# Performance work log

Hardware: AMD Instinct MI355X
Metric: run time of the kernel (lower is better)

The kernel has to match this reference:

```python
import jax, jax.numpy as jnp
import numpy as np
import math

N_HEAD = 32
ROPE_BASE = 10000.0


def _rope_headwise(x):
    # Faithful to the source bug: x is [B, H, S, D] and the rotary module uses
    # x.shape[1] (= H) as the "sequence length", so the angle depends on the
    # head index, broadcast over the true sequence axis.
    B, H, S, D = x.shape
    inv_freq = 1.0 / (ROPE_BASE ** (jnp.arange(0, D, 2, dtype=jnp.float32) / D))  # [D/2]
    t = jnp.arange(H, dtype=jnp.float32)                                          # [H]
    freqs = t[:, None] * inv_freq[None, :]                                        # [H, D/2]
    # emb = cat(freqs, freqs)[..., :D//2] == freqs, so cos/sin are just over freqs
    cos = jnp.cos(freqs)[None, :, None, :]   # [1, H, 1, D/2]
    sin = jnp.sin(freqs)[None, :, None, :]
    x1, x2 = x[..., : D // 2], x[..., D // 2 :]
    return jnp.concatenate([x1 * cos - x2 * sin, x1 * sin + x2 * cos], axis=-1)


def setup_inputs() -> dict:
    key = jax.random.key(0)
    ks = jax.random.split(key, 5)
    B, S, E = 2, 2048, 2048
    scale = 0.02
    return {
        "x": jax.random.normal(ks[0], (B, S, E), dtype=jnp.float32),
        "Wq": jax.random.normal(ks[1], (E, E), dtype=jnp.float32) * scale,
        "bq": jnp.zeros((E,), dtype=jnp.float32),
        "Wk": jax.random.normal(ks[2], (E, E), dtype=jnp.float32) * scale,
        "bk": jnp.zeros((E,), dtype=jnp.float32),
        "Wv": jax.random.normal(ks[3], (E, E), dtype=jnp.float32) * scale,
        "bv": jnp.zeros((E,), dtype=jnp.float32),
        "Wo": jax.random.normal(ks[4], (E, E), dtype=jnp.float32) * scale,
        "bo": jnp.zeros((E,), dtype=jnp.float32),
    }


def reference(x, Wq, bq, Wk, bk, Wv, bv, Wo, bo):
    B, S, E = x.shape
    H = N_HEAD
    D = E // H

    def split_heads(y):  # [B,S,E] -> [B,H,S,D]
        return y.reshape(B, S, H, D).transpose(0, 2, 1, 3)

    q = split_heads(x @ Wq + bq)
    k = split_heads(x @ Wk + bk)
    v = split_heads(x @ Wv + bv)

    q = _rope_headwise(q)
    k = _rope_headwise(k)

    scores = jnp.einsum("bhqd,bhkd->bhqk", q, k) / math.sqrt(D)  # [B,H,S,S]
    causal = jnp.triu(jnp.ones((S, S), dtype=bool), k=1)
    scores = jnp.where(causal[None, None], -jnp.inf, scores)
    attn = jax.nn.softmax(scores, axis=-1)
    out = jnp.einsum("bhqk,bhkd->bhqd", attn, v)                 # [B,H,S,D]
    out = out.transpose(0, 2, 1, 3).reshape(B, S, E)
    return out @ Wo + bo
```

## Files before the change

### kernel.cpp

```cpp
#include <hip/hip_runtime.h>
#include <hip/hip_bf16.h>

#define B_ 2
#define S_ 2048
#define E_ 2048
#define H_ 32
#define M_ (B_*S_)

typedef __bf16 bf16x8 __attribute__((ext_vector_type(8)));
typedef float  f32x4  __attribute__((ext_vector_type(4)));

__device__ __forceinline__ ushort f2bf(float f) {
    uint u = __float_as_uint(f);
    u += 0x7fffu + ((u >> 16) & 1u);
    return (ushort)(u >> 16);
}
__device__ __forceinline__ uint pack2bf(float a, float b) {
    __hip_bfloat162 h = __float22bfloat162_rn(make_float2(a, b));
    return *(uint*)&h;
}
__device__ __forceinline__ float bf2f(ushort h) {
    return __uint_as_float(((uint)h) << 16);
}
__device__ __forceinline__ f32x4 f4zero() {
    f32x4 z; z[0]=0.f; z[1]=0.f; z[2]=0.f; z[3]=0.f; return z;
}
__device__ __forceinline__ void async16(const ushort* g, ushort* l) {
    __builtin_amdgcn_global_load_lds((const __attribute__((address_space(1))) void*)g,
                                     (__attribute__((address_space(3))) void*)l, 16, 0, 0);
}

__global__ __launch_bounds__(256) void cast_x_kernel(const float* __restrict__ x,
                                                     ushort* __restrict__ xb) {
    int i = (blockIdx.x * 256 + threadIdx.x) * 4;
    float4 v = *(const float4*)(x + i);
    uint2 o;
    o.x = pack2bf(v.x, v.y);
    o.y = pack2bf(v.z, v.w);
    *(uint2*)(xb + i) = o;
}

__global__ __launch_bounds__(256) void wtrans_kernel(const float* __restrict__ W0, const float* __restrict__ W1,
                                                     const float* __restrict__ W2, const float* __restrict__ W3,
                                                     ushort* __restrict__ T0, ushort* __restrict__ T1,
                                                     ushort* __restrict__ T2, ushort* __restrict__ T3) {
    const float* W = (blockIdx.z==0)?W0:(blockIdx.z==1)?W1:(blockIdx.z==2)?W2:W3;
    ushort*      T = (blockIdx.z==0)?T0:(blockIdx.z==1)?T1:(blockIdx.z==2)?T2:T3;
    __shared__ float tile[64][65];
    const int k0 = blockIdx.y * 64, n0 = blockIdx.x * 64;
    const int rr = threadIdx.x >> 4;
    const int cc = (threadIdx.x & 15) * 4;
    #pragma unroll
    for (int p = 0; p < 4; ++p) {
        int r = p * 16 + rr;
        float4 v = *(const float4*)(W + (size_t)(k0 + r) * E_ + n0 + cc);
        tile[r][cc+0] = v.x; tile[r][cc+1] = v.y; tile[r][cc+2] = v.z; tile[r][cc+3] = v.w;
    }
    __syncthreads();
    #pragma unroll
    for (int p = 0; p < 4; ++p) {
        int rn = p * 16 + rr;
        uint2 o;
        o.x = pack2bf(tile[cc+0][rn], tile[cc+1][rn]);
        o.y = pack2bf(tile[cc+2][rn], tile[cc+3][rn]);
        *(uint2*)(T + (size_t)(n0 + rn) * E_ + k0 + cc) = o;
    }
}

__global__ __launch_bounds__(256) void vtrans_kernel(const ushort* __restrict__ vb,
                                                     ushort* __restrict__ vt) {
    __shared__ ushort tile[64][65];
    const int bh = blockIdx.y, b = bh >> 5, h = bh & 31;
    const int s0 = blockIdx.x * 64;
    int tx = threadIdx.x & 63, ty = threadIdx.x >> 6;
    #pragma unroll
    for (int it = 0; it < 16; ++it) {
        int r = it * 4 + ty;
        tile[r][tx] = vb[(size_t)(b * S_ + s0 + r) * E_ + h * 64 + tx];
    }
    __syncthreads();
    #pragma unroll
    for (int it = 0; it < 16; ++it) {
        int r = it * 4 + ty;
        vt[(size_t)(bh * 64 + r) * S_ + s0 + tx] = tile[tx][r];
    }
}

#define VMW4 asm volatile("s_waitcnt vmcnt(4)" ::: "memory")
#define VMW0 asm volatile("s_waitcnt vmcnt(0)" ::: "memory")
#define MEMB asm volatile("" ::: "memory")

#define STA_(bf, kt, h) { _Pragma("unroll") for (int it_ = 0; it_ < 2; ++it_) { \
    async16(A + (size_t)(m0 + it_*128 + (h)*64 + srow) * E_ + (kt)*64 + scg*8,  \
            &As[bf][(it_*128 + (h)*64 + wave*8) * 64]); } }

#define STB_(bf, kt, h) { _Pragma("unroll") for (int it_ = 0; it_ < 2; ++it_) { \
    int rih_ = it_*64 + srow;                                                   \
    int ldr_ = ((rih_ >> 5) << 6) + (h)*32 + (rih_ & 31);                       \
    int rwb_ = it_*64 + wave*8;                                                 \
    int wbs_ = ((rwb_ >> 5) << 6) + (h)*32 + (rwb_ & 31);                       \
    async16(Bt + (size_t)(n0 + ldr_) * E_ + (kt)*64 + scg*8,                    \
            &Bs[bf][wbs_ * 64]); } }

#define PHASE_(bf, mh, nh, STAGES) {                                            \
    bf16x8 paf[4][2], pbf[2][2];                                                \
    _Pragma("unroll") for (int m_ = 0; m_ < 4; ++m_)                            \
      _Pragma("unroll") for (int k_ = 0; k_ < 2; ++k_) {                        \
        int row_ = wm*128 + ((mh)*4 + m_)*16 + l15;                             \
        paf[m_][k_] = *(const bf16x8*)(&As[bf][row_*64 + (((k_*4 + quad) ^ (row_ & 7)) << 3)]); } \
    _Pragma("unroll") for (int n_ = 0; n_ < 2; ++n_)                            \
      _Pragma("unroll") for (int k_ = 0; k_ < 2; ++k_) {                        \
        int row_ = wn*64 + ((nh)*2 + n_)*16 + l15;                              \
        pbf[n_][k_] = *(const bf16x8*)(&Bs[bf][row_*64 + (((k_*4 + quad) ^ (row_ & 7)) << 3)]); } \
    STAGES;                                                                     \
    MEMB; __builtin_amdgcn_s_barrier();                                         \
    asm volatile("s_waitcnt lgkmcnt(0)" ::: "memory");                          \
    __builtin_amdgcn_sched_barrier(0);                                          \
    __builtin_amdgcn_s_setprio(1);                                              \
    _Pragma("unroll") for (int k_ = 0; k_ < 2; ++k_)                            \
      _Pragma("unroll") for (int m_ = 0; m_ < 4; ++m_)                          \
        _Pragma("unroll") for (int n_ = 0; n_ < 2; ++n_)                        \
          acc[(mh)*4+m_][(nh)*2+n_] = __builtin_amdgcn_mfma_f32_16x16x32_bf16(  \
              paf[m_][k_], pbf[n_][k_], acc[(mh)*4+m_][(nh)*2+n_], 0, 0, 0);    \
    __builtin_amdgcn_s_setprio(0);                                              \
    MEMB; __builtin_amdgcn_s_barrier(); MEMB;                                   \
  }

template<bool OUTF32, bool DOROPE, int NZ>
__global__ __launch_bounds__(512, 2) void gemm256(const ushort* __restrict__ A,
        const ushort* __restrict__ Bt0, const ushort* __restrict__ Bt1, const ushort* __restrict__ Bt2,
        const float* __restrict__ bias0, const float* __restrict__ bias1, const float* __restrict__ bias2,
        void* __restrict__ C0, void* __restrict__ C1, void* __restrict__ C2) {
    const int bid = blockIdx.x;
    const int z   = bid % NZ;
    const int nb  = (bid / NZ) % (E_ / 256);
    const int mb  = bid / (NZ * (E_ / 256));

    const ushort* Bt  = (z==0)?Bt0:(z==1)?Bt1:Bt2;
    const float* bias = (z==0)?bias0:(z==1)?bias1:bias2;
    void* Cv          = (z==0)?C0:(z==1)?C1:C2;

    __shared__ ushort As[2][256 * 64];
    __shared__ ushort Bs[2][256 * 64];

    const int tid  = threadIdx.x;
    const int wave = tid >> 6, lane = tid & 63;
    const int quad = lane >> 4, l15 = lane & 15;
    const int wm = wave >> 2, wn = wave & 3;
    const int m0 = mb * 256, n0 = nb * 256;
    const int srow = tid >> 3;
    const int scg  = (tid & 7) ^ (srow & 7);

    f32x4 acc[8][4];
    #pragma unroll
    for (int i = 0; i < 8; ++i)
        #pragma unroll
        for (int j = 0; j < 4; ++j) acc[i][j] = f4zero();

    STB_(0, 0, 1); STA_(0, 0, 1); STA_(0, 0, 0); STB_(0, 0, 0);
    STB_(1, 1, 1); STA_(1, 1, 1);
    VMW4;
    MEMB; __builtin_amdgcn_s_barrier(); MEMB;

    #pragma unroll 1
    for (int i = 0; i < 15; ++i) {
        const int t1 = 2*i + 1, t2 = 2*i + 2, t3 = 2*i + 3;
        PHASE_(0, 0, 1, STA_(1, t1, 0));
        PHASE_(0, 1, 1, STB_(1, t1, 0));
        PHASE_(0, 1, 0, STB_(0, t2, 1));
        PHASE_(0, 0, 0, STA_(0, t2, 1); VMW4);
        PHASE_(1, 0, 1, STA_(0, t2, 0));
        PHASE_(1, 1, 1, STB_(0, t2, 0));
        PHASE_(1, 1, 0, STB_(1, t3, 1));
        PHASE_(1, 0, 0, STA_(1, t3, 1); VMW4);
    }
    PHASE_(0, 0, 1, STA_(1, 31, 0));
    PHASE_(0, 1, 1, STB_(1, 31, 0));
    PHASE_(0, 1, 0, {});
    PHASE_(0, 0, 0, VMW0);
    PHASE_(1, 0, 1, {});
    PHASE_(1, 1, 1, {});
    PHASE_(1, 1, 0, {});
    PHASE_(1, 0, 0, {});

    if (DOROPE && z != 2) {
        const float qsc = (z == 0) ? 0.125f * 1.44269504f : 1.0f;
        const int h = (n0 + wn * 64) >> 6;
        float sn[2], cs[2];
        #pragma unroll
        for (int nt = 0; nt < 2; ++nt) {
            int j = nt * 16 + l15;
            float ang = (float)h * __expf(-(float)j * 0.28782313662425575f);
            __sincosf(ang, &sn[nt], &cs[nt]);
        }
        ushort* C = (ushort*)Cv;
        #pragma unroll
        for (int f = 0; f < 8; ++f) {
            #pragma unroll
            for (int nt = 0; nt < 2; ++nt) {
                int col1 = n0 + wn * 64 + nt * 16 + l15;
                float b1 = bias[col1], b2 = bias[col1 + 32];
                #pragma unroll
                for (int r = 0; r < 4; ++r) {
                    int rowg = m0 + wm * 128 + f * 16 + quad * 4 + r;
                    float x1 = acc[f][nt][r] + b1;
                    float x2 = acc[f][nt + 2][r] + b2;
                    C[(size_t)rowg * E_ + col1]      = f2bf((x1 * cs[nt] - x2 * sn[nt]) * qsc);
                    C[(size_t)rowg * E_ + col1 + 32] = f2bf((x1 * sn[nt] + x2 * cs[nt]) * qsc);
                }
            }
        }
    } else {
        #pragma unroll
        for (int f = 0; f < 8; ++f) {
            #pragma unroll
            for (int nt = 0; nt < 4; ++nt) {
                int col = n0 + wn * 64 + nt * 16 + l15;
                float bv = bias[col];
                #pragma unroll
                for (int r = 0; r < 4; ++r) {
                    int rowg = m0 + wm * 128 + f * 16 + quad * 4 + r;
                    float v = acc[f][nt][r] + bv;
                    if (OUTF32) ((float*)Cv)[(size_t)rowg * E_ + col] = v;
                    else        ((ushort*)Cv)[(size_t)rowg * E_ + col] = f2bf(v);
                }
            }
        }
    }
}
#undef STA_
#undef STB_
#undef PHASE_

template<bool OUTF32, bool DOROPE, int NZ>
__global__ __launch_bounds__(256) void gemm128(const ushort* __restrict__ A,
        const ushort* __restrict__ Bt0, const ushort* __restrict__ Bt1, const ushort* __restrict__ Bt2,
        const float* __restrict__ bias0, const float* __restrict__ bias1, const float* __restrict__ bias2,
        void* __restrict__ C0, void* __restrict__ C1, void* __restrict__ C2) {
    const int bid = blockIdx.x;
    const int z   = bid % NZ;
    const int nb  = (bid / NZ) % (E_ / 128);
    const int mb  = bid / (NZ * (E_ / 128));

    const ushort* Bt  = (z==0)?Bt0:(z==1)?Bt1:Bt2;
    const float* bias = (z==0)?bias0:(z==1)?bias1:bias2;
    void* Cv          = (z==0)?C0:(z==1)?C1:C2;

    __shared__ ushort As[128 * 64];
    __shared__ ushort Bs[128 * 64];

    const int tid  = threadIdx.x;
    const int wave = tid >> 6, lane = tid & 63;
    const int quad = lane >> 4, l15 = lane & 15;
    const int wm = wave >> 1, wn = wave & 1;
    const int m0 = mb * 128, n0 = nb * 128;
    const int srow = tid >> 3;
    const int scgx = (tid & 7) ^ (srow & 7);

    f32x4 acc[4][4];
    #pragma unroll
    for (int i = 0; i < 4; ++i)
        #pragma unroll
        for (int j = 0; j < 4; ++j) acc[i][j] = f4zero();

    for (int k0 = 0; k0 < E_; k0 += 64) {
        #pragma unroll
        for (int it = 0; it < 4; ++it) {
            int r = it * 32 + srow;
            async16(A  + (size_t)(m0 + r) * E_ + k0 + scgx * 8, As + (it * 256 + wave * 64) * 8);
            async16(Bt + (size_t)(n0 + r) * E_ + k0 + scgx * 8, Bs + (it * 256 + wave * 64) * 8);
        }
        __syncthreads();
        #pragma unroll
        for (int kk = 0; kk < 2; ++kk) {
            bf16x8 af[4], bfr[4];
            #pragma unroll
            for (int mt = 0; mt < 4; ++mt) {
                int row = wm * 64 + mt * 16 + l15;
                af[mt] = *(const bf16x8*)(As + row * 64 + (((kk * 4 + quad) ^ (row & 7)) << 3));
            }
            #pragma unroll
            for (int nt = 0; nt < 4; ++nt) {
                int row = wn * 64 + nt * 16 + l15;
                bfr[nt] = *(const bf16x8*)(Bs + row * 64 + (((kk * 4 + quad) ^ (row & 7)) << 3));
            }
            #pragma unroll
            for (int mt = 0; mt < 4; ++mt)
                #pragma unroll
                for (int nt = 0; nt < 4; ++nt)
                    acc[mt][nt] = __builtin_amdgcn_mfma_f32_16x16x32_bf16(af[mt], bfr[nt], acc[mt][nt], 0, 0, 0);
        }
        __syncthreads();
    }

    if (DOROPE && z != 2) {
        const float qsc = (z == 0) ? 0.125f * 1.44269504f : 1.0f;
        const int h = (n0 + wn * 64) >> 6;
        float sn[2], cs[2];
        #pragma unroll
        for (int nt = 0; nt < 2; ++nt) {
            int j = nt * 16 + l15;
            float ang = (float)h * __expf(-(float)j * 0.28782313662425575f);
            __sincosf(ang, &sn[nt], &cs[nt]);
        }
        ushort* C = (ushort*)Cv;
        #pragma unroll
        for (int mt = 0; mt < 4; ++mt) {
            #pragma unroll
            for (int nt = 0; nt < 2; ++nt) {
                int col1 = n0 + wn * 64 + nt * 16 + l15;
                float b1 = bias[col1], b2 = bias[col1 + 32];
                #pragma unroll
                for (int r = 0; r < 4; ++r) {
                    int rowg = m0 + wm * 64 + mt * 16 + quad * 4 + r;
                    float x1 = acc[mt][nt][r] + b1;
                    float x2 = acc[mt][nt + 2][r] + b2;
                    C[(size_t)rowg * E_ + col1]      = f2bf((x1 * cs[nt] - x2 * sn[nt]) * qsc);
                    C[(size_t)rowg * E_ + col1 + 32] = f2bf((x1 * sn[nt] + x2 * cs[nt]) * qsc);
                }
            }
        }
    } else {
        #pragma unroll
        for (int mt = 0; mt < 4; ++mt) {
            #pragma unroll
            for (int nt = 0; nt < 4; ++nt) {
                int col = n0 + wn * 64 + nt * 16 + l15;
                float bv = bias[col];
                #pragma unroll
                for (int r = 0; r < 4; ++r) {
                    int rowg = m0 + wm * 64 + mt * 16 + quad * 4 + r;
                    float v = acc[mt][nt][r] + bv;
                    if (OUTF32) ((float*)Cv)[(size_t)rowg * E_ + col] = v;
                    else        ((ushort*)Cv)[(size_t)rowg * E_ + col] = f2bf(v);
                }
            }
        }
    }
}

__global__ __launch_bounds__(256) void flash_kernel(const ushort* __restrict__ qb,
        const ushort* __restrict__ kb, const ushort* __restrict__ vt,
        ushort* __restrict__ ctx) {
    __shared__ ushort KVs[2][2][64 * 64];
    __shared__ ushort Ps[4][32 * 64];

    const int tid  = threadIdx.x;
    const int wave = tid >> 6, lane = tid & 63;
    const int quad = lane >> 4, l15 = lane & 15;
    const int bh = blockIdx.y, b = bh >> 5, h = bh & 31;
    const int srow = tid >> 3;
    const int scgx = (tid & 7) ^ (srow & 7);
    ushort* Pw = Ps[wave];

    bf16x8 ones;
    #pragma unroll
    for (int j = 0; j < 8; ++j) ones[j] = (__bf16)1.0f;

    #pragma unroll 1
    for (int pass = 0; pass < 2; ++pass) {
        const int qx  = pass ? (15 - (int)blockIdx.x) : (int)blockIdx.x;
        const int q0  = qx * 128;
        const int qw0 = q0 + wave * 32;
        const int nkt = 2 * qx + 2;

        bf16x8 qf[2][2];
        #pragma unroll
        for (int mt = 0; mt < 2; ++mt)
            #pragma unroll
            for (int kk = 0; kk < 2; ++kk)
                qf[mt][kk] = *(const bf16x8*)(qb + (size_t)(b * S_ + qw0 + mt * 16 + l15) * E_ + h * 64 + kk * 32 + quad * 8);

        f32x4 oacc[2][4], lacc[2];
        #pragma unroll
        for (int mt = 0; mt < 2; ++mt) {
            lacc[mt] = f4zero();
            #pragma unroll
            for (int dt = 0; dt < 4; ++dt) oacc[mt][dt] = f4zero();
        }

        #pragma unroll
        for (int it = 0; it < 2; ++it) {
            int r = it * 32 + srow;
            async16(kb + (size_t)(b * S_ + r) * E_ + h * 64 + scgx * 8, KVs[0][0] + (it * 256 + wave * 64) * 8);
            async16(vt + (size_t)(bh * 64 + r) * S_ + scgx * 8,         KVs[0][1] + (it * 256 + wave * 64) * 8);
        }
        __syncthreads();

        #pragma unroll 1
        for (int kt = 0; kt < nkt; ++kt) {
            const int k0 = kt * 64;
            if (kt + 1 < nkt) {
                const int kn = k0 + 64;
                ushort* Kd = KVs[(kt + 1) & 1][0];
                ushort* Vd = KVs[(kt + 1) & 1][1];
                #pragma unroll
                for (int it = 0; it < 2; ++it) {
                    int r = it * 32 + srow;
                    async16(kb + (size_t)(b * S_ + kn + r) * E_ + h * 64 + scgx * 8, Kd + (it * 256 + wave * 64) * 8);
                    async16(vt + (size_t)(bh * 64 + r) * S_ + kn + scgx * 8,         Vd + (it * 256 + wave * 64) * 8);
                }
            }

            if (k0 <= qw0 + 31) {
                const ushort* Ks = KVs[kt & 1][0];
                const ushort* Vs = KVs[kt & 1][1];
                f32x4 sacc[2][4];
                #pragma unroll
                for (int mt = 0; mt < 2; ++mt)
                    #pragma unroll
                    for (int nt = 0; nt < 4; ++nt) sacc[mt][nt] = f4zero();
                #pragma unroll
                for (int kk = 0; kk < 2; ++kk)
                    #pragma unroll
                    for (int nt = 0; nt < 4; ++nt) {
                        int row = nt * 16 + l15;
                        bf16x8 kf = *(const bf16x8*)(Ks + row * 64 + (((kk * 4 + quad) ^ (row & 7)) << 3));
                        #pragma unroll
                        for (int mt = 0; mt < 2; ++mt)
                            sacc[mt][nt] = __builtin_amdgcn_mfma_f32_16x16x32_bf16(kf, qf[mt][kk], sacc[mt][nt], 0, 0, 0);
                    }

                #pragma unroll
                for (int mt = 0; mt < 2; ++mt) {
                    const int q  = qw0 + mt * 16 + l15;
                    const bool dm = (k0 + 63 > qw0 + mt * 16);
                    const int ql = mt * 16 + l15, swz = ql & 7;
                    #pragma unroll
                    for (int nt = 0; nt < 4; ++nt) {
                        float p[4];
                        #pragma unroll
                        for (int r = 0; r < 4; ++r) {
                            int s = k0 + nt * 16 + quad * 4 + r;
                            p[r] = exp2f(sacc[mt][nt][r]);
                            if (dm && s > q) p[r] = 0.f;
                        }
                        uint2 pk;
                        pk.x = pack2bf(p[0], p[1]);
                        pk.y = pack2bf(p[2], p[3]);
                        *(uint2*)(Pw + ql * 64 + (((nt * 2 + (quad >> 1)) ^ swz) << 3) + (quad & 1) * 4) = pk;
                    }
                }

                #pragma unroll
                for (int kk = 0; kk < 2; ++kk) {
                    bf16x8 pf[2];
                    #pragma unroll
                    for (int mt = 0; mt < 2; ++mt) {
                        int ql = mt * 16 + l15;
                        pf[mt] = *(const bf16x8*)(Pw + ql * 64 + (((kk * 4 + quad) ^ (ql & 7)) << 3));
                    }
                    #pragma unroll
                    for (int mt = 0; mt < 2; ++mt)
                        lacc[mt] = __builtin_amdgcn_mfma_f32_16x16x32_bf16(pf[mt], ones, lacc[mt], 0, 0, 0);
                    #pragma unroll
                    for (int dt = 0; dt < 4; ++dt) {
                        int row = dt * 16 + l15;
                        bf16x8 vf = *(const bf16x8*)(Vs + row * 64 + (((kk * 4 + quad) ^ (row & 7)) << 3));
                        #pragma unroll
                        for (int mt = 0; mt < 2; ++mt)
                            oacc[mt][dt] = __builtin_amdgcn_mfma_f32_16x16x32_bf16(pf[mt], vf, oacc[mt][dt], 0, 0, 0);
                    }
                }
            }
            __syncthreads();
        }

        #pragma unroll
        for (int mt = 0; mt < 2; ++mt)
            #pragma unroll
            for (int r = 0; r < 4; ++r) {
                float inv = 1.0f / lacc[mt][r];
                #pragma unroll
                for (int dt = 0; dt < 4; ++dt)
                    ctx[(size_t)(b * S_ + qw0 + mt * 16 + quad * 4 + r) * E_ + h * 64 + dt * 16 + l15] =
                        f2bf(oacc[mt][dt][r] * inv);
            }
    }
}

extern "C" void kernel_launch(void* const* d_in, const int* in_sizes, int n_in,
                              void* d_out, int out_size, void* d_ws, size_t ws_size,
                              hipStream_t stream) {
    const float* x  = (const float*)d_in[0];
    const float* Wq = (const float*)d_in[1];
    const float* bq = (const float*)d_in[2];
    const float* Wk = (const float*)d_in[3];
    const float* bk = (const float*)d_in[4];
    const float* Wv = (const float*)d_in[5];
    const float* bv = (const float*)d_in[6];
    const float* Wo = (const float*)d_in[7];
    const float* bo = (const float*)d_in[8];
    float* out = (float*)d_out;

    ushort* p   = (ushort*)d_ws;
    ushort* xb  = p; p += (size_t)M_ * E_;
    ushort* wqt = p; p += (size_t)E_ * E_;
    ushort* wkt = p; p += (size_t)E_ * E_;
    ushort* wvt = p; p += (size_t)E_ * E_;
    ushort* wot = p; p += (size_t)E_ * E_;
    ushort* qb  = p; p += (size_t)M_ * E_;
    ushort* kb  = p; p += (size_t)M_ * E_;
    ushort* vb  = p; p += (size_t)M_ * E_;
    ushort* ctx = p; p += (size_t)M_ * E_;
    ushort* vt  = xb;

    cast_x_kernel<<<(M_ * E_) / 1024, 256, 0, stream>>>(x, xb);
    wtrans_kernel<<<dim3(E_ / 64, E_ / 64, 4), 256, 0, stream>>>(Wq, Wk, Wv, Wo, wqt, wkt, wvt, wot);
    gemm256<false, true, 3><<<(E_ / 256) * (M_ / 256) * 3, 512, 0, stream>>>(
        xb, wqt, wkt, wvt, bq, bk, bv, qb, kb, vb);
    vtrans_kernel<<<dim3(S_ / 64, B_ * H_), 256, 0, stream>>>(vb, vt);
    flash_kernel<<<dim3(8, B_ * H_), 256, 0, stream>>>(qb, kb, vt, ctx);
    gemm128<true, false, 1><<<(E_ / 128) * (M_ / 128), 256, 0, stream>>>(
        ctx, wot, wot, wot, bo, bo, bo, out, out, out);
}
```

Measured before the change: 443.6 us.

## Reuse LDS fragments across phases with serpentine quadrant order in GEMM loop

The per-phase quadrant order becomes a serpentine walk ((0,1),(0,0),(1,0),(1,1)), so consecutive phases share either the A or the B fragment. Fragments live in registers across phases and only the changed operand is reloaded from LDS. The global-to-LDS stage order is reshuffled to match which half of the tile is consumed and when. This roughly halves LDS reads per k-tile, at the cost of keeping more fragment registers live across barriers, which risks register pressure at two blocks per CU.

After: 409.9 us. -7.6%, faster.

```diff
diff --git a/kernel.cpp b/kernel.cpp
--- a/kernel.cpp
+++ b/kernel.cpp
@@ -102,16 +102,17 @@
     async16(Bt + (size_t)(n0 + ldr_) * E_ + (kt)*64 + scg*8,                    \
             &Bs[bf][wbs_ * 64]); } }
 
-#define PHASE_(bf, mh, nh, STAGES) {                                            \
-    bf16x8 paf[4][2], pbf[2][2];                                                \
-    _Pragma("unroll") for (int m_ = 0; m_ < 4; ++m_)                            \
-      _Pragma("unroll") for (int k_ = 0; k_ < 2; ++k_) {                        \
-        int row_ = wm*128 + ((mh)*4 + m_)*16 + l15;                             \
-        paf[m_][k_] = *(const bf16x8*)(&As[bf][row_*64 + (((k_*4 + quad) ^ (row_ & 7)) << 3)]); } \
-    _Pragma("unroll") for (int n_ = 0; n_ < 2; ++n_)                            \
-      _Pragma("unroll") for (int k_ = 0; k_ < 2; ++k_) {                        \
-        int row_ = wn*64 + ((nh)*2 + n_)*16 + l15;                              \
-        pbf[n_][k_] = *(const bf16x8*)(&Bs[bf][row_*64 + (((k_*4 + quad) ^ (row_ & 7)) << 3)]); } \
+#define PHASE_(bf, mh, nh, LA, LB, STAGES) {                                    \
+    if (LA) {                                                                   \
+      _Pragma("unroll") for (int m_ = 0; m_ < 4; ++m_)                          \
+        _Pragma("unroll") for (int k_ = 0; k_ < 2; ++k_) {                      \
+          int row_ = wm*128 + ((mh)*4 + m_)*16 + l15;                           \
+          pa[m_][k_] = *(const bf16x8*)(&As[bf][row_*64 + (((k_*4 + quad) ^ (row_ & 7)) << 3)]); } } \
+    if (LB) {                                                                   \
+      _Pragma("unroll") for (int n_ = 0; n_ < 2; ++n_)                          \
+        _Pragma("unroll") for (int k_ = 0; k_ < 2; ++k_) {                      \
+          int row_ = wn*64 + ((nh)*2 + n_)*16 + l15;                            \
+          pb[n_][k_] = *(const bf16x8*)(&Bs[bf][row_*64 + (((k_*4 + quad) ^ (row_ & 7)) << 3)]); } } \
     STAGES;                                                                     \
     MEMB; __builtin_amdgcn_s_barrier();                                         \
     asm volatile("s_waitcnt lgkmcnt(0)" ::: "memory");                          \
@@ -121,7 +122,7 @@
       _Pragma("unroll") for (int m_ = 0; m_ < 4; ++m_)                          \
         _Pragma("unroll") for (int n_ = 0; n_ < 2; ++n_)                        \
           acc[(mh)*4+m_][(nh)*2+n_] = __builtin_amdgcn_mfma_f32_16x16x32_bf16(  \
-              paf[m_][k_], pbf[n_][k_], acc[(mh)*4+m_][(nh)*2+n_], 0, 0, 0);    \
+              pa[m_][k_], pb[n_][k_], acc[(mh)*4+m_][(nh)*2+n_], 0, 0, 0);      \
     __builtin_amdgcn_s_setprio(0);                                              \
     MEMB; __builtin_amdgcn_s_barrier(); MEMB;                                   \
   }
@@ -157,31 +158,33 @@
         #pragma unroll
         for (int j = 0; j < 4; ++j) acc[i][j] = f4zero();
 
-    STB_(0, 0, 1); STA_(0, 0, 1); STA_(0, 0, 0); STB_(0, 0, 0);
-    STB_(1, 1, 1); STA_(1, 1, 1);
+    bf16x8 pa[4][2], pb[2][2];
+
+    STA_(0, 0, 0); STA_(0, 0, 1); STB_(0, 0, 0); STB_(0, 0, 1);
+    STA_(1, 1, 0); STB_(1, 1, 0);
     VMW4;
     MEMB; __builtin_amdgcn_s_barrier(); MEMB;
 
     #pragma unroll 1
     for (int i = 0; i < 15; ++i) {
         const int t1 = 2*i + 1, t2 = 2*i + 2, t3 = 2*i + 3;
-        PHASE_(0, 0, 1, STA_(1, t1, 0));
-        PHASE_(0, 1, 1, STB_(1, t1, 0));
-        PHASE_(0, 1, 0, STB_(0, t2, 1));
-        PHASE_(0, 0, 0, STA_(0, t2, 1); VMW4);
-        PHASE_(1, 0, 1, STA_(0, t2, 0));
-        PHASE_(1, 1, 1, STB_(0, t2, 0));
-        PHASE_(1, 1, 0, STB_(1, t3, 1));
-        PHASE_(1, 0, 0, STA_(1, t3, 1); VMW4);
-    }
-    PHASE_(0, 0, 1, STA_(1, 31, 0));
-    PHASE_(0, 1, 1, STB_(1, 31, 0));
-    PHASE_(0, 1, 0, {});
-    PHASE_(0, 0, 0, VMW0);
-    PHASE_(1, 0, 1, {});
-    PHASE_(1, 1, 1, {});
-    PHASE_(1, 1, 0, {});
-    PHASE_(1, 0, 0, {});
+        PHASE_(0, 0, 1, 1, 1, STB_(1, t1, 1));
+        PHASE_(0, 0, 0, 0, 1, STA_(1, t1, 1));
+        PHASE_(0, 1, 0, 1, 0, STA_(0, t2, 0));
+        PHASE_(0, 1, 1, 0, 1, STB_(0, t2, 0); VMW4);
+        PHASE_(1, 0, 1, 1, 1, STB_(0, t2, 1));
+        PHASE_(1, 0, 0, 0, 1, STA_(0, t2, 1));
+        PHASE_(1, 1, 0, 1, 0, STA_(1, t3, 0));
+        PHASE_(1, 1, 1, 0, 1, STB_(1, t3, 0); VMW4);
+    }
+    PHASE_(0, 0, 1, 1, 1, STB_(1, 31, 1));
+    PHASE_(0, 0, 0, 0, 1, STA_(1, 31, 1));
+    PHASE_(0, 1, 0, 1, 0, {});
+    PHASE_(0, 1, 1, 0, 1, VMW0);
+    PHASE_(1, 0, 1, 1, 1, {});
+    PHASE_(1, 0, 0, 0, 1, {});
+    PHASE_(1, 1, 0, 1, 0, {});
+    PHASE_(1, 1, 1, 0, 1, {});
 
     if (DOROPE && z != 2) {
         const float qsc = (z == 0) ? 0.125f * 1.44269504f : 1.0f;
```
